# Kernel tuning notes

Measured on AMD Instinct MI355X. Metric: run time of the kernel, lower is better.

## Reference

```python
import jax, jax.numpy as jnp
import numpy as np

N_NODES = 100000
N_EDGES = 800000
N_GRAPHS = 64
D_IN = 128
D_H = 256
D_MID = 64
D_OUT = 3


def _sage_conv(x, src, dst, Wl, bl, Wr, n_nodes):
    # PyG SAGEConv (mean aggr): out = lin_l(mean_{j in N(i)} x_j) + lin_r(x_i)
    msg_sum = jax.ops.segment_sum(x[src], dst, num_segments=n_nodes)   # [N, d]
    deg = jax.ops.segment_sum(jnp.ones((src.shape[0],), x.dtype), dst,
                              num_segments=n_nodes)                     # [N]
    mean = msg_sum / jnp.maximum(deg, 1.0)[:, None]
    return mean @ Wl + bl + x @ Wr


def setup_inputs() -> dict:
    key = jax.random.key(0)
    ks = jax.random.split(key, 16)
    s = 0.05
    inp = {
        "x": jax.random.normal(ks[0], (N_NODES, D_IN), dtype=jnp.float32),
        "edge_index": jax.random.randint(ks[1], (2, N_EDGES), 0, N_NODES, dtype=jnp.int32),
        "batch": jnp.sort(jax.random.randint(ks[2], (N_NODES,), 0, N_GRAPHS, dtype=jnp.int32)),
        # conv1
        "W1l": jax.random.normal(ks[3], (D_IN, D_H), dtype=jnp.float32) * s,
        "b1l": jnp.zeros((D_H,), jnp.float32),
        "W1r": jax.random.normal(ks[4], (D_IN, D_H), dtype=jnp.float32) * s,
        # conv2
        "W2l": jax.random.normal(ks[5], (D_H, D_H), dtype=jnp.float32) * s,
        "b2l": jnp.zeros((D_H,), jnp.float32),
        "W2r": jax.random.normal(ks[6], (D_H, D_H), dtype=jnp.float32) * s,
        # conv3
        "W3l": jax.random.normal(ks[7], (D_H, D_H), dtype=jnp.float32) * s,
        "b3l": jnp.zeros((D_H,), jnp.float32),
        "W3r": jax.random.normal(ks[8], (D_H, D_H), dtype=jnp.float32) * s,
        # head
        "Wlin1": jax.random.normal(ks[9], (D_H, D_MID), dtype=jnp.float32) * s,
        "blin1": jnp.zeros((D_MID,), jnp.float32),
        "Wlin2": jax.random.normal(ks[10], (D_MID, D_OUT), dtype=jnp.float32) * s,
        "blin2": jnp.zeros((D_OUT,), jnp.float32),
    }
    return inp


def reference(x, edge_index, batch, W1l, b1l, W1r, W2l, b2l, W2r,
              W3l, b3l, W3r, Wlin1, blin1, Wlin2, blin2):
    src, dst = edge_index[0], edge_index[1]
    h = jnp.tanh(_sage_conv(x, src, dst, W1l, b1l, W1r, N_NODES))
    h = jnp.tanh(_sage_conv(h, src, dst, W2l, b2l, W2r, N_NODES))
    h = _sage_conv(h, src, dst, W3l, b3l, W3r, N_NODES)
    pooled = jax.ops.segment_max(h, batch, num_segments=N_GRAPHS)  # [G, 256]
    pooled = jnp.where(jnp.isneginf(pooled), 0.0, pooled)  # empty segments -> 0
    # dropout_rate = 0.0 -> identity
    h = jnp.tanh(pooled @ Wlin1 + blin1)
    return h @ Wlin2 + blin2
```

## Files before the change

kernel.cpp:

```cpp
#include <hip/hip_runtime.h>

#define N_NODES 100000
#define N_PAD   100224
#define N_EDGES 800000
#define N_GRAPHS 64
#define D_IN 128
#define D_H 256

typedef __attribute__((ext_vector_type(8))) short bf16x8;
typedef __attribute__((ext_vector_type(8))) unsigned short u16x8;
typedef __attribute__((ext_vector_type(4))) float f32x4;

__device__ inline float bf2f(unsigned short u) {
    union { unsigned u32; float f; } x;
    x.u32 = ((unsigned)u) << 16;
    return x.f;
}
__device__ inline unsigned short f2bf(float f) {
    unsigned u = __float_as_uint(f);
    if ((u & 0x7fffffffu) > 0x7f800000u) return (unsigned short)0x7fc0;
    unsigned r = ((u >> 16) & 1u) + 0x7fffu;
    return (unsigned short)((u + r) >> 16);
}

__device__ inline unsigned enc_f32(float f) {
    unsigned u = __float_as_uint(f);
    return (u & 0x80000000u) ? ~u : (u | 0x80000000u);
}
__device__ inline float dec_f32(unsigned u) {
    unsigned v = (u & 0x80000000u) ? (u & 0x7FFFFFFFu) : ~u;
    return __uint_as_float(v);
}
#define ENC_NEG_INF 0x007FFFFFu

#define GLOAD_LDS16(g, l)                                                     \
    __builtin_amdgcn_global_load_lds(                                         \
        (const __attribute__((address_space(1))) unsigned int*)(g),           \
        (__attribute__((address_space(3))) unsigned int*)(l), 16, 0, 0)

__global__ void k_init_counts(int* __restrict__ counts) {
    int i = blockIdx.x * blockDim.x + threadIdx.x;
    if (i < N_NODES) counts[i] = 0;
}

__global__ void k_count(const int* __restrict__ dst, int* __restrict__ counts) {
    int e = blockIdx.x * blockDim.x + threadIdx.x;
    if (e < N_EDGES) atomicAdd(&counts[dst[e]], 1);
}

__global__ void k_scan_block(const int* __restrict__ counts, int* __restrict__ excl,
                             int* __restrict__ bsums) {
    __shared__ int sh[1024];
    int tid = threadIdx.x;
    int i = blockIdx.x * 1024 + tid;
    int v = (i < N_NODES) ? counts[i] : 0;
    sh[tid] = v;
    __syncthreads();
    for (int off = 1; off < 1024; off <<= 1) {
        int t = (tid >= off) ? sh[tid - off] : 0;
        __syncthreads();
        sh[tid] += t;
        __syncthreads();
    }
    if (i < N_NODES) excl[i] = sh[tid] - v;
    if (tid == 1023) bsums[blockIdx.x] = sh[1023];
}

__global__ void k_scan_top(int* __restrict__ bsums, int nb) {
    __shared__ int sh[128];
    int tid = threadIdx.x;
    int v = (tid < nb) ? bsums[tid] : 0;
    sh[tid] = v;
    __syncthreads();
    for (int off = 1; off < 128; off <<= 1) {
        int t = (tid >= off) ? sh[tid - off] : 0;
        __syncthreads();
        sh[tid] += t;
        __syncthreads();
    }
    if (tid < nb) bsums[tid] = sh[tid] - v;
}

__global__ void k_scan_finish(const int* __restrict__ excl, const int* __restrict__ bsums,
                              const int* __restrict__ counts, int* __restrict__ indptr,
                              int* __restrict__ cursor, float* __restrict__ deg_inv,
                              unsigned* __restrict__ pooled) {
    int i = blockIdx.x * blockDim.x + threadIdx.x;
    if (i < N_GRAPHS * 256) pooled[i] = ENC_NEG_INF;
    if (i < N_NODES) {
        int p = excl[i] + bsums[i >> 10];
        indptr[i] = p;
        cursor[i] = p;
        deg_inv[i] = 1.0f / fmaxf((float)counts[i], 1.0f);
        if (i == 0) indptr[N_NODES] = N_EDGES;
    }
}

__global__ void k_fill(const int* __restrict__ src, const int* __restrict__ dst,
                       int* __restrict__ cursor, int* __restrict__ eidx) {
    int e = blockIdx.x * blockDim.x + threadIdx.x;
    if (e < N_EDGES) {
        int pos = atomicAdd(&cursor[dst[e]], 1);
        eidx[pos] = src[e];
    }
}

__global__ void k_x2bf(const float* __restrict__ x, unsigned short* __restrict__ hx) {
    const int total = N_NODES * D_IN / 4;
    for (int i = blockIdx.x * blockDim.x + threadIdx.x; i < total;
         i += gridDim.x * blockDim.x) {
        float4 v = reinterpret_cast<const float4*>(x)[i];
        ushort4 o;
        o.x = f2bf(v.x); o.y = f2bf(v.y); o.z = f2bf(v.z); o.w = f2bf(v.w);
        reinterpret_cast<ushort4*>(hx)[i] = o;
    }
}

__global__ void k_wt_all(const float* __restrict__ W1l, const float* __restrict__ W1r,
                         const float* __restrict__ W2l, const float* __restrict__ W2r,
                         const float* __restrict__ W3l, const float* __restrict__ W3r,
                         unsigned short* __restrict__ T1l, unsigned short* __restrict__ T1r,
                         unsigned short* __restrict__ T2l, unsigned short* __restrict__ T2r,
                         unsigned short* __restrict__ T3l, unsigned short* __restrict__ T3r) {
    const int S1 = 128 * 256, S2 = 256 * 256;
    const int total = 2 * S1 + 4 * S2;
    for (int idx = blockIdx.x * blockDim.x + threadIdx.x; idx < total;
         idx += gridDim.x * blockDim.x) {
        const float* W; unsigned short* T; int i, K;
        if (idx < S1)           { W = W1l; T = T1l; i = idx;            K = 128; }
        else if (idx < 2 * S1)  { W = W1r; T = T1r; i = idx - S1;       K = 128; }
        else if (idx < 2*S1+S2) { W = W2l; T = T2l; i = idx - 2*S1;     K = 256; }
        else if (idx < 2*S1+2*S2) { W = W2r; T = T2r; i = idx-2*S1-S2;  K = 256; }
        else if (idx < 2*S1+3*S2) { W = W3l; T = T3l; i = idx-2*S1-2*S2; K = 256; }
        else                    { W = W3r; T = T3r; i = idx-2*S1-3*S2;  K = 256; }
        int k = i >> 8, n = i & 255;
        T[n * K + k] = f2bf(W[(size_t)k * 256 + n]);
    }
}

template <bool IN_F32>
__global__ void k_agg(const void* __restrict__ hin, const int* __restrict__ indptr,
                      const int* __restrict__ eidx, const float* __restrict__ deg_inv,
                      unsigned short* __restrict__ mean) {
    constexpr int D = IN_F32 ? 128 : 256;
    constexpr int CA = IN_F32 ? 8 : 16;
    int wid = (blockIdx.x * blockDim.x + threadIdx.x) >> 6;
    int lane = threadIdx.x & 63;
    int nw = (gridDim.x * blockDim.x) >> 6;
    int g = lane >> 4;
    int l16 = lane & 15;
    for (int node = wid; node < N_NODES; node += nw) {
        int beg = indptr[node], end = indptr[node + 1];
        float acc[CA] = {};
        for (int e = beg + g; e < end; e += 4) {
            int s = eidx[e];
            if (IN_F32) {
                const float4* row = reinterpret_cast<const float4*>((const float*)hin + (size_t)s * D);
                float4 v0 = row[l16 * 2], v1 = row[l16 * 2 + 1];
                acc[0] += v0.x; acc[1] += v0.y; acc[2] += v0.z; acc[3] += v0.w;
                acc[4] += v1.x; acc[5] += v1.y; acc[6] += v1.z; acc[7] += v1.w;
            } else {
                const u16x8* row = reinterpret_cast<const u16x8*>((const unsigned short*)hin + (size_t)s * D);
                u16x8 v0 = row[l16 * 2], v1 = row[l16 * 2 + 1];
#pragma unroll
                for (int j = 0; j < 8; ++j) acc[j] += bf2f((unsigned short)v0[j]);
#pragma unroll
                for (int j = 0; j < 8; ++j) acc[8 + j] += bf2f((unsigned short)v1[j]);
            }
        }
#pragma unroll
        for (int i = 0; i < CA; ++i) {
            acc[i] += __shfl_xor(acc[i], 16);
            acc[i] += __shfl_xor(acc[i], 32);
        }
        if (g == 0) {
            float inv = deg_inv[node];
            unsigned short* orow = mean + (size_t)node * (IN_F32 ? 128 : 256);
            if (IN_F32) {
                u16x8 o;
#pragma unroll
                for (int j = 0; j < 8; ++j) o[j] = f2bf(acc[j] * inv);
                reinterpret_cast<u16x8*>(orow)[l16] = o;
            } else {
                u16x8 o0, o1;
#pragma unroll
                for (int j = 0; j < 8; ++j) o0[j] = f2bf(acc[j] * inv);
#pragma unroll
                for (int j = 0; j < 8; ++j) o1[j] = f2bf(acc[8 + j] * inv);
                reinterpret_cast<u16x8*>(orow)[l16 * 2] = o0;
                reinterpret_cast<u16x8*>(orow)[l16 * 2 + 1] = o1;
            }
        }
    }
}

template <int K, bool TANH, bool POOL>
__global__ __launch_bounds__(512)
void k_xform(const unsigned short* __restrict__ A0, const unsigned short* __restrict__ A1,
             const unsigned short* __restrict__ Bt0, const unsigned short* __restrict__ Bt1,
             const float* __restrict__ bias,
             unsigned short* __restrict__ out,
             const int* __restrict__ batch, unsigned* __restrict__ pooled) {
    __shared__ unsigned short Al[128 * 32];
    __shared__ unsigned short Bl[256 * 32];

    const int tid = threadIdx.x;
    const int lane = tid & 63;
    const int wid = tid >> 6;
    const int wr = wid >> 1 >> 1;
    const int wc = wid & 3;
    const int m0 = blockIdx.x * 128;

    const int srow = lane >> 2;
    const int schunk = (lane & 3) ^ ((lane >> 3) & 3);
    const int koffs = schunk * 8;

    f32x4 acc[4][4] = {};

#pragma unroll
    for (int slab = 0; slab < 2; ++slab) {
        const unsigned short* As = slab ? A1 : A0;
        const unsigned short* Bs = slab ? Bt1 : Bt0;
        for (int k0 = 0; k0 < K; k0 += 32) {
            __syncthreads();
            GLOAD_LDS16(As + (size_t)(m0 + wid * 16 + srow) * K + k0 + koffs,
                        &Al[wid * 512]);
#pragma unroll
            for (int cc = 0; cc < 2; ++cc) {
                int c = wid * 2 + cc;
                GLOAD_LDS16(Bs + (size_t)(c * 16 + srow) * K + k0 + koffs,
                            &Bl[c * 512]);
            }
            asm volatile("s_waitcnt vmcnt(0)" ::: "memory");
            __syncthreads();

            bf16x8 af[4], bfr[4];
#pragma unroll
            for (int f = 0; f < 4; ++f) {
                int ra = wr * 64 + f * 16 + (lane & 15);
                int pa = ((lane >> 4) ^ ((ra >> 1) & 3)) * 8;
                af[f] = *reinterpret_cast<const bf16x8*>(&Al[ra * 32 + pa]);
                int rb = wc * 64 + f * 16 + (lane & 15);
                int pb = ((lane >> 4) ^ ((rb >> 1) & 3)) * 8;
                bfr[f] = *reinterpret_cast<const bf16x8*>(&Bl[rb * 32 + pb]);
            }
#pragma unroll
            for (int fi = 0; fi < 4; ++fi)
#pragma unroll
                for (int fj = 0; fj < 4; ++fj)
                    acc[fi][fj] = __builtin_amdgcn_mfma_f32_16x16x32_bf16(
                        af[fi], bfr[fj], acc[fi][fj], 0, 0, 0);
        }
    }

    const int rbase = m0 + wr * 64 + (lane >> 4) * 4;
    const int cbase = wc * 64 + (lane & 15);
    if (POOL) {
#pragma unroll
        for (int fj = 0; fj < 4; ++fj) {
            int col = cbase + fj * 16;
            float bcol = bias[col];
            int curg = -1;
            float curmax = 0.f;
#pragma unroll
            for (int fi = 0; fi < 4; ++fi) {
#pragma unroll
                for (int r = 0; r < 4; ++r) {
                    int row = rbase + fi * 16 + r;
                    if (row >= N_NODES) continue;
                    float v = acc[fi][fj][r] + bcol;
                    if (TANH) v = tanhf(v);
                    int g = batch[row];
                    if (g != curg) {
                        if (curg >= 0) atomicMax(&pooled[curg * 256 + col], enc_f32(curmax));
                        curg = g;
                        curmax = v;
                    } else {
                        curmax = fmaxf(curmax, v);
                    }
                }
            }
            if (curg >= 0) atomicMax(&pooled[curg * 256 + col], enc_f32(curmax));
        }
    } else {
#pragma unroll
        for (int fi = 0; fi < 4; ++fi) {
#pragma unroll
            for (int fj = 0; fj < 4; ++fj) {
                int col = cbase + fj * 16;
                float bcol = bias[col];
#pragma unroll
                for (int r = 0; r < 4; ++r) {
                    int row = rbase + fi * 16 + r;
                    if (row >= N_NODES) continue;
                    float v = acc[fi][fj][r] + bcol;
                    if (TANH) v = tanhf(v);
                    out[(size_t)row * 256 + col] = f2bf(v);
                }
            }
        }
    }
}

__global__ void k_head(const unsigned* __restrict__ pooled,
                       const float* __restrict__ W1, const float* __restrict__ b1,
                       const float* __restrict__ W2, const float* __restrict__ b2,
                       float* __restrict__ out) {
    __shared__ float p[256];
    __shared__ float hm[64];
    int g = blockIdx.x;
    int t = threadIdx.x;
    for (int k = t; k < 256; k += 64) {
        unsigned u = pooled[g * 256 + k];
        p[k] = (u == ENC_NEG_INF) ? 0.0f : dec_f32(u);
    }
    __syncthreads();
    float a = b1[t];
    for (int k = 0; k < 256; ++k) a += p[k] * W1[k * 64 + t];
    hm[t] = tanhf(a);
    __syncthreads();
    if (t < 3) {
        float o = b2[t];
        for (int m = 0; m < 64; ++m) o += hm[m] * W2[m * 3 + t];
        out[g * 3 + t] = o;
    }
}

extern "C" void kernel_launch(void* const* d_in, const int* in_sizes, int n_in,
                              void* d_out, int out_size, void* d_ws, size_t ws_size,
                              hipStream_t stream) {
    const float* x     = (const float*)d_in[0];
    const int*   ei    = (const int*)d_in[1];
    const int*   src   = ei;
    const int*   dst   = ei + N_EDGES;
    const int*   batch = (const int*)d_in[2];
    const float* W1l = (const float*)d_in[3];
    const float* b1l = (const float*)d_in[4];
    const float* W1r = (const float*)d_in[5];
    const float* W2l = (const float*)d_in[6];
    const float* b2l = (const float*)d_in[7];
    const float* W2r = (const float*)d_in[8];
    const float* W3l = (const float*)d_in[9];
    const float* b3l = (const float*)d_in[10];
    const float* W3r = (const float*)d_in[11];
    const float* Wlin1 = (const float*)d_in[12];
    const float* blin1 = (const float*)d_in[13];
    const float* Wlin2 = (const float*)d_in[14];
    const float* blin2 = (const float*)d_in[15];
    float* out = (float*)d_out;

    char* base = (char*)d_ws;
    size_t off = 0;
    auto alloc = [&](size_t bytes) { char* p = base + off; off += (bytes + 255) & ~(size_t)255; return (void*)p; };
    int*   counts  = (int*)alloc(N_NODES * 4);
    int*   indptr  = (int*)alloc((N_NODES + 1) * 4);
    int*   cursor  = (int*)alloc(N_NODES * 4);
    int*   excl    = (int*)alloc(N_NODES * 4);
    int*   bsums   = (int*)alloc(128 * 4);
    float* deg_inv = (float*)alloc(N_NODES * 4);
    unsigned* pooled = (unsigned*)alloc(N_GRAPHS * 256 * 4);
    int*   eidx    = (int*)alloc(N_EDGES * 4);
    unsigned short* Wt1l = (unsigned short*)alloc(256 * 128 * 2);
    unsigned short* Wt1r = (unsigned short*)alloc(256 * 128 * 2);
    unsigned short* Wt2l = (unsigned short*)alloc(256 * 256 * 2);
    unsigned short* Wt2r = (unsigned short*)alloc(256 * 256 * 2);
    unsigned short* Wt3l = (unsigned short*)alloc(256 * 256 * 2);
    unsigned short* Wt3r = (unsigned short*)alloc(256 * 256 * 2);
    unsigned short* M   = (unsigned short*)alloc((size_t)N_PAD * 256 * 2);
    unsigned short* hA  = (unsigned short*)alloc((size_t)N_PAD * 256 * 2);
    unsigned short* hxB = (unsigned short*)alloc((size_t)N_PAD * 256 * 2);
    unsigned short* hx = hxB;
    unsigned short* hB = hxB;

    const int NB_SCAN = (N_NODES + 1023) / 1024;

    k_init_counts<<<(N_NODES + 255) / 256, 256, 0, stream>>>(counts);
    k_count<<<(N_EDGES + 255) / 256, 256, 0, stream>>>(dst, counts);
    k_scan_block<<<NB_SCAN, 1024, 0, stream>>>(counts, excl, bsums);
    k_scan_top<<<1, 128, 0, stream>>>(bsums, NB_SCAN);
    k_scan_finish<<<(N_NODES + 255) / 256, 256, 0, stream>>>(excl, bsums, counts, indptr, cursor, deg_inv, pooled);
    k_fill<<<(N_EDGES + 255) / 256, 256, 0, stream>>>(src, dst, cursor, eidx);

    k_x2bf<<<2048, 256, 0, stream>>>(x, hx);
    k_wt_all<<<1280, 256, 0, stream>>>(W1l, W1r, W2l, W2r, W3l, W3r,
                                       Wt1l, Wt1r, Wt2l, Wt2r, Wt3l, Wt3r);

    dim3 ggrid(782);

    k_agg<true><<<2048, 256, 0, stream>>>(x, indptr, eidx, deg_inv, M);
    k_xform<128, true, false><<<ggrid, 512, 0, stream>>>(M, hx, Wt1l, Wt1r, b1l, hA, nullptr, nullptr);

    k_agg<false><<<2048, 256, 0, stream>>>(hA, indptr, eidx, deg_inv, M);
    k_xform<256, true, false><<<ggrid, 512, 0, stream>>>(M, hA, Wt2l, Wt2r, b2l, hB, nullptr, nullptr);

    k_agg<false><<<2048, 256, 0, stream>>>(hB, indptr, eidx, deg_inv, M);
    k_xform<256, false, true><<<ggrid, 512, 0, stream>>>(M, hB, Wt3l, Wt3r, b3l, nullptr, batch, pooled);

    k_head<<<N_GRAPHS, 64, 0, stream>>>(pooled, Wlin1, blin1, Wlin2, blin2, out);
}
```

Baseline: 514.8 us.

## Double-buffer A tile in LDS and stream weights directly into registers in xform GEMM

Rewrites the node-transform GEMM to use 64-row blocks of 4 waves instead of 128-row blocks of 8 waves. The A tile is now double-buffered in LDS so the next k-slice loads while MFMAs run on the current one, with a single barrier per step. Weight fragments are read straight from global/L2 into registers and are no longer staged in LDS. This aims to hide load latency and cut barrier stalls, at the cost of more redundant weight reads per block and twice as many blocks.

```diff
diff --git a/kernel.cpp b/kernel.cpp
--- a/kernel.cpp
+++ b/kernel.cpp
@@ -195,65 +195,87 @@
 }
 
 template <int K, bool TANH, bool POOL>
-__global__ __launch_bounds__(512)
+__global__ __launch_bounds__(256)
 void k_xform(const unsigned short* __restrict__ A0, const unsigned short* __restrict__ A1,
              const unsigned short* __restrict__ Bt0, const unsigned short* __restrict__ Bt1,
              const float* __restrict__ bias,
              unsigned short* __restrict__ out,
              const int* __restrict__ batch, unsigned* __restrict__ pooled) {
-    __shared__ unsigned short Al[128 * 32];
-    __shared__ unsigned short Bl[256 * 32];
+    __shared__ unsigned short Al[2][64 * 32];
 
     const int tid = threadIdx.x;
     const int lane = tid & 63;
-    const int wid = tid >> 6;
-    const int wr = wid >> 1 >> 1;
-    const int wc = wid & 3;
-    const int m0 = blockIdx.x * 128;
+    const int wc = tid >> 6;
+    const int m0 = blockIdx.x * 64;
+
+    const int KS = K / 32;
+    const int NT = 2 * KS;
 
     const int srow = lane >> 2;
-    const int schunk = (lane & 3) ^ ((lane >> 3) & 3);
-    const int koffs = schunk * 8;
+    const int koffs = ((lane & 3) ^ ((lane >> 3) & 3)) * 8;
+    const int brow = lane & 15;
+    const int bk = (lane >> 4) * 8;
 
     f32x4 acc[4][4] = {};
 
-#pragma unroll
-    for (int slab = 0; slab < 2; ++slab) {
-        const unsigned short* As = slab ? A1 : A0;
-        const unsigned short* Bs = slab ? Bt1 : Bt0;
-        for (int k0 = 0; k0 < K; k0 += 32) {
-            __syncthreads();
-            GLOAD_LDS16(As + (size_t)(m0 + wid * 16 + srow) * K + k0 + koffs,
-                        &Al[wid * 512]);
-#pragma unroll
-            for (int cc = 0; cc < 2; ++cc) {
-                int c = wid * 2 + cc;
-                GLOAD_LDS16(Bs + (size_t)(c * 16 + srow) * K + k0 + koffs,
-                            &Bl[c * 512]);
-            }
-            asm volatile("s_waitcnt vmcnt(0)" ::: "memory");
-            __syncthreads();
-
-            bf16x8 af[4], bfr[4];
-#pragma unroll
-            for (int f = 0; f < 4; ++f) {
-                int ra = wr * 64 + f * 16 + (lane & 15);
-                int pa = ((lane >> 4) ^ ((ra >> 1) & 3)) * 8;
-                af[f] = *reinterpret_cast<const bf16x8*>(&Al[ra * 32 + pa]);
-                int rb = wc * 64 + f * 16 + (lane & 15);
-                int pb = ((lane >> 4) ^ ((rb >> 1) & 3)) * 8;
-                bfr[f] = *reinterpret_cast<const bf16x8*>(&Bl[rb * 32 + pb]);
-            }
-#pragma unroll
-            for (int fi = 0; fi < 4; ++fi)
-#pragma unroll
-                for (int fj = 0; fj < 4; ++fj)
-                    acc[fi][fj] = __builtin_amdgcn_mfma_f32_16x16x32_bf16(
-                        af[fi], bfr[fj], acc[fi][fj], 0, 0, 0);
-        }
-    }
-
-    const int rbase = m0 + wr * 64 + (lane >> 4) * 4;
+    auto stage = [&](int buf, int t) {
+        const unsigned short* As = (t < KS) ? A0 : A1;
+        int k0 = (t < KS ? t : t - KS) * 32;
+        GLOAD_LDS16(As + (size_t)(m0 + wc * 16 + srow) * K + k0 + koffs,
+                    &Al[buf][wc * 512]);
+    };
+    auto loadB = [&](bf16x8* b, int t) {
+        const unsigned short* Bs = (t < KS) ? Bt0 : Bt1;
+        int k0 = (t < KS ? t : t - KS) * 32;
+#pragma unroll
+        for (int f = 0; f < 4; ++f)
+            b[f] = *reinterpret_cast<const bf16x8*>(
+                Bs + (size_t)(wc * 64 + f * 16 + brow) * K + k0 + bk);
+    };
+    auto compute = [&](int buf, const bf16x8* b) {
+        bf16x8 af[4];
+#pragma unroll
+        for (int f = 0; f < 4; ++f) {
+            int ra = f * 16 + (lane & 15);
+            int pa = ((lane >> 4) ^ ((ra >> 1) & 3)) * 8;
+            af[f] = *reinterpret_cast<const bf16x8*>(&Al[buf][ra * 32 + pa]);
+        }
+#pragma unroll
+        for (int fi = 0; fi < 4; ++fi)
+#pragma unroll
+            for (int fj = 0; fj < 4; ++fj)
+                acc[fi][fj] = __builtin_amdgcn_mfma_f32_16x16x32_bf16(
+                    af[fi], b[fj], acc[fi][fj], 0, 0, 0);
+    };
+
+    bf16x8 bA[4], bB[4];
+
+    stage(0, 0);
+    __builtin_amdgcn_sched_barrier(0);
+    loadB(bA, 0);
+    asm volatile("s_waitcnt vmcnt(4)" ::: "memory");
+    __builtin_amdgcn_s_barrier();
+
+    for (int t = 0; t < NT; t += 2) {
+        stage(1, t + 1);
+        __builtin_amdgcn_sched_barrier(0);
+        loadB(bB, t + 1);
+        compute(0, bA);
+        asm volatile("s_waitcnt vmcnt(4) lgkmcnt(0)" ::: "memory");
+        __builtin_amdgcn_s_barrier();
+        if (t + 2 < NT) {
+            stage(0, t + 2);
+            __builtin_amdgcn_sched_barrier(0);
+            loadB(bA, t + 2);
+            compute(1, bB);
+            asm volatile("s_waitcnt vmcnt(4) lgkmcnt(0)" ::: "memory");
+            __builtin_amdgcn_s_barrier();
+        } else {
+            compute(1, bB);
+        }
+    }
+
+    const int rbase = m0 + (lane >> 4) * 4;
     const int cbase = wc * 64 + (lane & 15);
     if (POOL) {
 #pragma unroll
@@ -385,16 +407,16 @@
     k_wt_all<<<1280, 256, 0, stream>>>(W1l, W1r, W2l, W2r, W3l, W3r,
                                        Wt1l, Wt1r, Wt2l, Wt2r, Wt3l, Wt3r);
 
-    dim3 ggrid(782);
+    dim3 ggrid(N_PAD / 64);
 
     k_agg<true><<<2048, 256, 0, stream>>>(x, indptr, eidx, deg_inv, M);
-    k_xform<128, true, false><<<ggrid, 512, 0, stream>>>(M, hx, Wt1l, Wt1r, b1l, hA, nullptr, nullptr);
+    k_xform<128, true, false><<<ggrid, 256, 0, stream>>>(M, hx, Wt1l, Wt1r, b1l, hA, nullptr, nullptr);
 
     k_agg<false><<<2048, 256, 0, stream>>>(hA, indptr, eidx, deg_inv, M);
-    k_xform<256, true, false><<<ggrid, 512, 0, stream>>>(M, hA, Wt2l, Wt2r, b2l, hB, nullptr, nullptr);
+    k_xform<256, true, false><<<ggrid, 256, 0, stream>>>(M, hA, Wt2l, Wt2r, b2l, hB, nullptr, nullptr);
 
     k_agg<false><<<2048, 256, 0, stream>>>(hB, indptr, eidx, deg_inv, M);
-    k_xform<256, false, true><<<ggrid, 512, 0, stream>>>(M, hB, Wt3l, Wt3r, b3l, nullptr, batch, pooled);
+    k_xform<256, false, true><<<ggrid, 256, 0, stream>>>(M, hB, Wt3l, Wt3r, b3l, nullptr, batch, pooled);
 
     k_head<<<N_GRAPHS, 64, 0, stream>>>(pooled, Wlin1, blin1, Wlin2, blin2, out);
 }
```

Result: slower. 612.7 us (+19.0%).

## Stage per-block edge lists in LDS and gather layer-1 from bf16 input

Applied to the files above, without the earlier changes.

The aggregation kernel now gives each block a contiguous range of 64 nodes. Each block stages that range's CSR pointers and edge indices into shared memory, replacing the grid-stride, wave-per-node scheme. The first layer gathers from the bf16 copy of x instead of the fp32 input, halving the bytes per neighbour row. The bf16 gather can change numerics slightly, and blocks with more than 1152 edges fall back to global index loads.

```diff
diff --git a/kernel.cpp b/kernel.cpp
--- a/kernel.cpp
+++ b/kernel.cpp
@@ -138,55 +138,76 @@
     }
 }
 
-template <bool IN_F32>
-__global__ void k_agg(const void* __restrict__ hin, const int* __restrict__ indptr,
-                      const int* __restrict__ eidx, const float* __restrict__ deg_inv,
-                      unsigned short* __restrict__ mean) {
-    constexpr int D = IN_F32 ? 128 : 256;
-    constexpr int CA = IN_F32 ? 8 : 16;
-    int wid = (blockIdx.x * blockDim.x + threadIdx.x) >> 6;
-    int lane = threadIdx.x & 63;
-    int nw = (gridDim.x * blockDim.x) >> 6;
-    int g = lane >> 4;
-    int l16 = lane & 15;
-    for (int node = wid; node < N_NODES; node += nw) {
-        int beg = indptr[node], end = indptr[node + 1];
+template <int D>
+__global__ __launch_bounds__(256)
+void k_agg(const unsigned short* __restrict__ hin, const int* __restrict__ indptr,
+           const int* __restrict__ eidx, const float* __restrict__ deg_inv,
+           unsigned short* __restrict__ mean) {
+    constexpr int NB = 64;
+    constexpr int ECAP = 1152;
+    constexpr int CA = (D == 128) ? 8 : 16;
+    __shared__ int sptr[NB + 1];
+    __shared__ int sedge[ECAP];
+
+    const int n0 = blockIdx.x * NB;
+    const int tid = threadIdx.x;
+
+    if (tid <= NB) {
+        int n = n0 + tid;
+        sptr[tid] = indptr[n < N_NODES ? n : N_NODES];
+    }
+    __syncthreads();
+    const int ebeg = sptr[0];
+    const int ecnt = sptr[NB] - ebeg;
+    const int estaged = ecnt < ECAP ? ecnt : ECAP;
+    for (int i = tid; i < estaged; i += 256) sedge[i] = eidx[ebeg + i];
+    __syncthreads();
+
+    const int wv = tid >> 6;
+    const int lane = tid & 63;
+    const int g = lane >> 4;
+    const int l16 = lane & 15;
+
+    for (int i = 0; i < 16; ++i) {
+        int ln = wv * 16 + i;
+        int node = n0 + ln;
+        if (node >= N_NODES) break;
+        int b = sptr[ln] - ebeg, e = sptr[ln + 1] - ebeg;
         float acc[CA] = {};
-        for (int e = beg + g; e < end; e += 4) {
-            int s = eidx[e];
-            if (IN_F32) {
-                const float4* row = reinterpret_cast<const float4*>((const float*)hin + (size_t)s * D);
-                float4 v0 = row[l16 * 2], v1 = row[l16 * 2 + 1];
-                acc[0] += v0.x; acc[1] += v0.y; acc[2] += v0.z; acc[3] += v0.w;
-                acc[4] += v1.x; acc[5] += v1.y; acc[6] += v1.z; acc[7] += v1.w;
+        for (int j = b + g; j < e; j += 4) {
+            int s = (j < ECAP) ? sedge[j] : eidx[ebeg + j];
+            const u16x8* row = reinterpret_cast<const u16x8*>(hin + (size_t)s * D);
+            if (D == 128) {
+                u16x8 v = row[l16];
+#pragma unroll
+                for (int c = 0; c < 8; ++c) acc[c] += bf2f((unsigned short)v[c]);
             } else {
-                const u16x8* row = reinterpret_cast<const u16x8*>((const unsigned short*)hin + (size_t)s * D);
                 u16x8 v0 = row[l16 * 2], v1 = row[l16 * 2 + 1];
 #pragma unroll
-                for (int j = 0; j < 8; ++j) acc[j] += bf2f((unsigned short)v0[j]);
-#pragma unroll
-                for (int j = 0; j < 8; ++j) acc[8 + j] += bf2f((unsigned short)v1[j]);
-            }
-        }
-#pragma unroll
-        for (int i = 0; i < CA; ++i) {
-            acc[i] += __shfl_xor(acc[i], 16);
-            acc[i] += __shfl_xor(acc[i], 32);
+                for (int c = 0; c < 8; ++c) acc[c] += bf2f((unsigned short)v0[c]);
+#pragma unroll
+                for (int c = 0; c < 8; ++c) acc[8 + c] += bf2f((unsigned short)v1[c]);
+            }
+        }
+#pragma unroll
+        for (int c = 0; c < CA; ++c) {
+            acc[c] += __shfl_xor(acc[c], 16);
+            acc[c] += __shfl_xor(acc[c], 32);
         }
         if (g == 0) {
             float inv = deg_inv[node];
-            unsigned short* orow = mean + (size_t)node * (IN_F32 ? 128 : 256);
-            if (IN_F32) {
+            unsigned short* orow = mean + (size_t)node * D;
+            if (D == 128) {
                 u16x8 o;
 #pragma unroll
-                for (int j = 0; j < 8; ++j) o[j] = f2bf(acc[j] * inv);
+                for (int c = 0; c < 8; ++c) o[c] = f2bf(acc[c] * inv);
                 reinterpret_cast<u16x8*>(orow)[l16] = o;
             } else {
                 u16x8 o0, o1;
 #pragma unroll
-                for (int j = 0; j < 8; ++j) o0[j] = f2bf(acc[j] * inv);
-#pragma unroll
-                for (int j = 0; j < 8; ++j) o1[j] = f2bf(acc[8 + j] * inv);
+                for (int c = 0; c < 8; ++c) o0[c] = f2bf(acc[c] * inv);
+#pragma unroll
+                for (int c = 0; c < 8; ++c) o1[c] = f2bf(acc[8 + c] * inv);
                 reinterpret_cast<u16x8*>(orow)[l16 * 2] = o0;
                 reinterpret_cast<u16x8*>(orow)[l16 * 2 + 1] = o1;
             }
@@ -207,13 +228,12 @@
     const int tid = threadIdx.x;
     const int lane = tid & 63;
     const int wid = tid >> 6;
-    const int wr = wid >> 1 >> 1;
+    const int wr = wid >> 2;
     const int wc = wid & 3;
     const int m0 = blockIdx.x * 128;
 
     const int srow = lane >> 2;
-    const int schunk = (lane & 3) ^ ((lane >> 3) & 3);
-    const int koffs = schunk * 8;
+    const int koffs = ((lane & 3) ^ ((lane >> 3) & 3)) * 8;
 
     f32x4 acc[4][4] = {};
 
@@ -373,6 +393,7 @@
     unsigned short* hB = hxB;
 
     const int NB_SCAN = (N_NODES + 1023) / 1024;
+    const int NB_AGG = (N_NODES + 63) / 64;
 
     k_init_counts<<<(N_NODES + 255) / 256, 256, 0, stream>>>(counts);
     k_count<<<(N_EDGES + 255) / 256, 256, 0, stream>>>(dst, counts);
@@ -387,13 +408,13 @@
 
     dim3 ggrid(782);
 
-    k_agg<true><<<2048, 256, 0, stream>>>(x, indptr, eidx, deg_inv, M);
+    k_agg<128><<<NB_AGG, 256, 0, stream>>>(hx, indptr, eidx, deg_inv, M);
     k_xform<128, true, false><<<ggrid, 512, 0, stream>>>(M, hx, Wt1l, Wt1r, b1l, hA, nullptr, nullptr);
 
-    k_agg<false><<<2048, 256, 0, stream>>>(hA, indptr, eidx, deg_inv, M);
+    k_agg<256><<<NB_AGG, 256, 0, stream>>>(hA, indptr, eidx, deg_inv, M);
     k_xform<256, true, false><<<ggrid, 512, 0, stream>>>(M, hA, Wt2l, Wt2r, b2l, hB, nullptr, nullptr);
 
-    k_agg<false><<<2048, 256, 0, stream>>>(hB, indptr, eidx, deg_inv, M);
+    k_agg<256><<<NB_AGG, 256, 0, stream>>>(hB, indptr, eidx, deg_inv, M);
     k_xform<256, false, true><<<ggrid, 512, 0, stream>>>(M, hB, Wt3l, Wt3r, b3l, nullptr, batch, pooled);
 
     k_head<<<N_GRAPHS, 64, 0, stream>>>(pooled, Wlin1, blin1, Wlin2, blin2, out);
```

Result: faster. 500.5 us (-2.8%).
